# Kernel optimization log

Hardware: AMD Instinct MI355X
Metric: run time of the kernel (lower is better)

The kernel has to match this reference:

```python
import jax, jax.numpy as jnp
import numpy as np

B, T, D = 4, 2048, 768
H = 12
DH = D // H
DFF = 3072
EPS = 1e-5


def _layernorm(x, g, b):
    mu = jnp.mean(x, axis=-1, keepdims=True)
    var = jnp.var(x, axis=-1, keepdims=True)
    return (x - mu) * jax.lax.rsqrt(var + EPS) * g + b


def setup_inputs() -> dict:
    key = jax.random.key(0)
    ks = jax.random.split(key, 12)
    s = lambda fan_in: 1.0 / np.sqrt(fan_in)
    return {
        "x": jax.random.normal(ks[0], (B, T, D), dtype=jnp.float32),
        "ln1_g": jnp.ones((D,), jnp.float32),
        "ln1_b": jnp.zeros((D,), jnp.float32),
        "w_qkv": jax.random.uniform(ks[1], (D, 3 * D), jnp.float32, -s(D), s(D)),
        "b_qkv": jax.random.uniform(ks[2], (3 * D,), jnp.float32, -s(D), s(D)),
        "w_proj": jax.random.uniform(ks[3], (D, D), jnp.float32, -s(D), s(D)),
        "b_proj": jax.random.uniform(ks[4], (D,), jnp.float32, -s(D), s(D)),
        "ln2_g": jnp.ones((D,), jnp.float32),
        "ln2_b": jnp.zeros((D,), jnp.float32),
        "w_ff1": jax.random.uniform(ks[5], (D, DFF), jnp.float32, -s(D), s(D)),
        "b_ff1": jax.random.uniform(ks[6], (DFF,), jnp.float32, -s(D), s(D)),
        "w_ff2": jax.random.uniform(ks[7], (DFF, D), jnp.float32, -s(DFF), s(DFF)),
        "b_ff2": jax.random.uniform(ks[8], (D,), jnp.float32, -s(DFF), s(DFF)),
    }


def reference(x, ln1_g, ln1_b, w_qkv, b_qkv, w_proj, b_proj,
              ln2_g, ln2_b, w_ff1, b_ff1, w_ff2, b_ff2):
    # --- attention sublayer ---
    h = _layernorm(x, ln1_g, ln1_b)
    qkv = h @ w_qkv + b_qkv                       # [B,T,3D]
    q, k, v = jnp.split(qkv, 3, axis=-1)
    q = q.reshape(B, T, H, DH).transpose(0, 2, 1, 3)  # [B,H,T,DH]
    k = k.reshape(B, T, H, DH).transpose(0, 2, 1, 3)
    v = v.reshape(B, T, H, DH).transpose(0, 2, 1, 3)
    att = jnp.einsum('bhqd,bhkd->bhqk', q, k) / jnp.sqrt(jnp.float32(DH))
    causal = jnp.tril(jnp.ones((T, T), dtype=bool))
    att = jnp.where(causal, att, -jnp.inf)
    att = jax.nn.softmax(att, axis=-1)
    out = jnp.einsum('bhqk,bhkd->bhqd', att, v)    # [B,H,T,DH]
    out = out.transpose(0, 2, 1, 3).reshape(B, T, D)
    x = x + out @ w_proj + b_proj
    # --- MLP sublayer ---
    h2 = _layernorm(x, ln2_g, ln2_b)
    h2 = jax.nn.gelu(h2 @ w_ff1 + b_ff1, approximate=False)
    x = x + h2 @ w_ff2 + b_ff2
    return x
```

## Files before the change

### kernel.cpp

```cpp
#include <hip/hip_runtime.h>
#include <cstdint>
#include <cstddef>

typedef unsigned short u16;
typedef unsigned int u32;
typedef __attribute__((ext_vector_type(8))) short s16x8;
typedef __attribute__((ext_vector_type(4))) float f32x4;

#define NB 4
#define NT 2048
#define ND 768
#define NH 12
#define NDH 64
#define NFF 3072
#define NM (NB*NT)

__device__ __forceinline__ u16 f2b(float f){
  union { float f; unsigned u; } c; c.f = f;
  unsigned r = c.u + 0x7fffu + ((c.u >> 16) & 1u);
  return (u16)(r >> 16);
}

__device__ __forceinline__ f32x4 mfma16(s16x8 a, s16x8 b, f32x4 c){
  return __builtin_amdgcn_mfma_f32_16x16x32_bf16(a, b, c, 0, 0, 0);
}

__device__ __forceinline__ void stage16(u16* lds, const u16* g){
  __builtin_amdgcn_global_load_lds(
      (const __attribute__((address_space(1))) unsigned int*)g,
      (__attribute__((address_space(3))) unsigned int*)lds,
      16, 0, 0);
}

__device__ __forceinline__ float gelu_f(float v){
  const float x = v * 0.70710678118654752f;
  const float ax = fabsf(x);
  const float t = 1.f / (1.f + 0.3275911f * ax);
  const float y = t * (0.254829592f + t * (-0.284496736f + t * (1.421413741f
                + t * (-1.453152027f + t * 1.061405429f))));
  float er = 1.f - y * __expf(-ax * ax);
  er = copysignf(er, x);
  return 0.5f * v * (1.f + er);
}

__global__ __launch_bounds__(256) void transpose_bf16(
    const float* __restrict__ in, u16* __restrict__ out, int K, int N)
{
  __shared__ float tile[32][33];
  const int n0 = blockIdx.x * 32, k0 = blockIdx.y * 32;
  const int tx = threadIdx.x, ty = threadIdx.y;
  #pragma unroll
  for (int i = 0; i < 32; i += 8)
    tile[ty + i][tx] = in[(size_t)(k0 + ty + i) * N + n0 + tx];
  __syncthreads();
  #pragma unroll
  for (int i = 0; i < 32; i += 8)
    out[(size_t)(n0 + ty + i) * K + k0 + tx] = f2b(tile[tx][ty + i]);
}

__global__ __launch_bounds__(256) void ln_kernel(
    const float* __restrict__ x, const float* __restrict__ g,
    const float* __restrict__ b, u16* __restrict__ out)
{
  const int row = blockIdx.x;
  const int t = threadIdx.x;
  const float* xr = x + (size_t)row * ND;
  float v0 = xr[t], v1 = xr[t + 256], v2 = xr[t + 512];
  float s = v0 + v1 + v2;
  float ss = v0*v0 + v1*v1 + v2*v2;
  #pragma unroll
  for (int o = 32; o; o >>= 1) { s += __shfl_xor(s, o, 64); ss += __shfl_xor(ss, o, 64); }
  __shared__ float red[8];
  const int w = t >> 6;
  if ((t & 63) == 0) { red[w] = s; red[4 + w] = ss; }
  __syncthreads();
  s  = red[0] + red[1] + red[2] + red[3];
  ss = red[4] + red[5] + red[6] + red[7];
  const float mu = s * (1.f / ND);
  const float var = ss * (1.f / ND) - mu * mu;
  const float rinv = rsqrtf(var + 1e-5f);
  u16* orow = out + (size_t)row * ND;
  orow[t]       = f2b((v0 - mu) * rinv * g[t]       + b[t]);
  orow[t + 256] = f2b((v1 - mu) * rinv * g[t + 256] + b[t + 256]);
  orow[t + 512] = f2b((v2 - mu) * rinv * g[t + 512] + b[t + 512]);
}

template<int EPI>
__global__ __launch_bounds__(512,6) void gemm_bt(
    const u16* __restrict__ A, const u16* __restrict__ Bt,
    const float* __restrict__ bias, const float* __restrict__ res,
    void* __restrict__ o0, void* __restrict__ o1, void* __restrict__ o2,
    const int M, const int N, const int K)
{
  __shared__ u16 As[128 * 32];
  __shared__ u16 Bs[128 * 32];
  const int tid = threadIdx.x;
  const int lane = tid & 63, wid = tid >> 6;
  const int wr = wid >> 1, wc = wid & 1;
  const int lg = lane >> 4, lm = lane & 15;

  const int nwg = gridDim.x * gridDim.y;
  int bid = blockIdx.y * gridDim.x + blockIdx.x;
  bid = (bid & 7) * (nwg >> 3) + (bid >> 3);
  const int bm = (bid & 63) * 128, bn = (bid >> 6) * 128;

  f32x4 acc[2][4] = {};

  const int srow = tid >> 2;
  const int schunk = (tid & 3) ^ ((tid >> 3) & 3);
  const u16* ApT = A  + (size_t)(bm + srow) * K + schunk * 8;
  const u16* BpT = Bt + (size_t)(bn + srow) * K + schunk * 8;
  const int woff = wid * 512;
  const int fswz = (lm >> 1) & 3;

  const int nt = K >> 5;
  for (int t = 0; t < nt; ++t) {
    const int k0 = t << 5;
    __syncthreads();
    stage16(&As[woff], ApT + k0);
    stage16(&Bs[woff], BpT + k0);
    __syncthreads();
    s16x8 af[2], bf[4];
    #pragma unroll
    for (int i = 0; i < 2; i++)
      af[i] = *(const s16x8*)&As[(wr * 32 + i * 16 + lm) * 32 + ((lg ^ fswz) * 8)];
    #pragma unroll
    for (int j = 0; j < 4; j++)
      bf[j] = *(const s16x8*)&Bs[(wc * 64 + j * 16 + lm) * 32 + ((lg ^ fswz) * 8)];
    #pragma unroll
    for (int i = 0; i < 2; i++)
      #pragma unroll
      for (int j = 0; j < 4; j++)
        acc[i][j] = mfma16(af[i], bf[j], acc[i][j]);
  }

  #pragma unroll
  for (int i = 0; i < 2; i++)
    #pragma unroll
    for (int j = 0; j < 4; j++) {
      const int col = bn + wc * 64 + j * 16 + lm;
      const float bb = bias[col];
      #pragma unroll
      for (int r = 0; r < 4; r++) {
        const int row = bm + wr * 32 + i * 16 + lg * 4 + r;
        float v = acc[i][j][r] + bb;
        if (EPI == 0) {
          u16* dst; int rem;
          if (col < ND)            { dst = (u16*)o0; rem = col; v *= 0.125f; }
          else if (col < 2 * ND)   { dst = (u16*)o1; rem = col - ND; }
          else                     { dst = (u16*)o2; rem = col - 2 * ND; }
          const int hh = rem >> 6, dh = rem & 63;
          const int bb2 = row >> 11, tt = row & 2047;
          dst[(((size_t)bb2 * NH + hh) * NT + tt) * NDH + dh] = f2b(v);
        } else if (EPI == 1) {
          ((float*)o0)[(size_t)row * ND + col] = v + res[(size_t)row * ND + col];
        } else if (EPI == 2) {
          ((u16*)o0)[(size_t)row * NFF + col] = f2b(gelu_f(v));
        } else {
          ((float*)o0)[(size_t)row * ND + col] = v + res[(size_t)row * ND + col];
        }
      }
    }
}

__global__ __launch_bounds__(256,2) void attn_kernel(
    const u16* __restrict__ Q, const u16* __restrict__ Kg,
    const u16* __restrict__ V, u16* __restrict__ O)
{
  const int pairIdx = blockIdx.x;
  const int bh = blockIdx.y;
  const int b = bh / NH, h = bh % NH;
  const int tid = threadIdx.x;
  const int lane = tid & 63, w = tid >> 6;
  const int lg = lane >> 4, lm = lane & 15;
  const int sr = tid >> 3;
  const int sc = (tid & 7) * 8;

  __shared__ u16 Ks[64 * 64];
  __shared__ u16 Vt[64 * 64];
  __shared__ u16 Ps[4][16 * 64];

  const u16* Qb = Q  + (size_t)bh * NT * NDH;
  const u16* Kb = Kg + (size_t)bh * NT * NDH;
  const u16* Vb = V  + (size_t)bh * NT * NDH;

  for (int half = 0; half < 2; ++half) {
    const int si = half ? (31 - pairIdx) : pairIdx;
    const int q0 = si * 64;
    const int ktmax = si;

    const s16x8 qf0 = *(const s16x8*)&Qb[(size_t)(q0 + w * 16 + lm) * NDH + lg * 8];
    const s16x8 qf1 = *(const s16x8*)&Qb[(size_t)(q0 + w * 16 + lm) * NDH + 32 + lg * 8];

    f32x4 oacc[4] = {};
    float m = -INFINITY, l = 0.f;

    s16x8 kva = *(const s16x8*)&Kb[(size_t)sr * NDH + sc];
    s16x8 kvb = *(const s16x8*)&Kb[(size_t)(sr + 32) * NDH + sc];
    s16x8 vva = *(const s16x8*)&Vb[(size_t)sr * NDH + sc];
    s16x8 vvb = *(const s16x8*)&Vb[(size_t)(sr + 32) * NDH + sc];

    for (int kt = 0; kt <= ktmax; ++kt) {
      __syncthreads();
      *(s16x8*)&Ks[sr * 64 + (sc ^ ((sr & 7) << 3))] = kva;
      *(s16x8*)&Ks[(sr + 32) * 64 + (sc ^ ((sr & 7) << 3))] = kvb;
      #pragma unroll
      for (int e = 0; e < 8; ++e)
        Vt[(sc + e) * 64 + (sr ^ ((tid & 7) << 3))] = (u16)vva[e];
      #pragma unroll
      for (int e = 0; e < 8; ++e)
        Vt[(sc + e) * 64 + ((sr + 32) ^ ((tid & 7) << 3))] = (u16)vvb[e];
      __syncthreads();

      if (kt < ktmax) {
        const u16* Kn = Kb + (size_t)(kt + 1) * 64 * NDH;
        const u16* Vn = Vb + (size_t)(kt + 1) * 64 * NDH;
        kva = *(const s16x8*)&Kn[(size_t)sr * NDH + sc];
        kvb = *(const s16x8*)&Kn[(size_t)(sr + 32) * NDH + sc];
        vva = *(const s16x8*)&Vn[(size_t)sr * NDH + sc];
        vvb = *(const s16x8*)&Vn[(size_t)(sr + 32) * NDH + sc];
      }

      f32x4 sv[4];
      #pragma unroll
      for (int n = 0; n < 4; ++n) {
        const int krow = (n * 16 + lm) * 64;
        const int swz = (lm & 7) << 3;
        s16x8 kf0 = *(const s16x8*)&Ks[krow + ((lg * 8) ^ swz)];
        s16x8 kf1 = *(const s16x8*)&Ks[krow + ((32 + lg * 8) ^ swz)];
        f32x4 s4 = {};
        s4 = mfma16(kf0, qf0, s4);
        s4 = mfma16(kf1, qf1, s4);
        sv[n] = s4;
      }

      if (kt == ktmax) {
        #pragma unroll
        for (int n = 0; n < 4; ++n)
          #pragma unroll
          for (int r = 0; r < 4; ++r)
            if (n * 16 + lg * 4 + r > w * 16 + lm) sv[n][r] = -INFINITY;
      }

      float mx = -INFINITY;
      #pragma unroll
      for (int n = 0; n < 4; ++n)
        #pragma unroll
        for (int r = 0; r < 4; ++r) mx = fmaxf(mx, sv[n][r]);
      mx = fmaxf(mx, __shfl_xor(mx, 16));
      mx = fmaxf(mx, __shfl_xor(mx, 32));
      const float mnew = fmaxf(m, mx);
      const float alpha = __expf(m - mnew);
      m = mnew;

      float rs = 0.f;
      u32 pk[4][2];
      #pragma unroll
      for (int n = 0; n < 4; ++n) {
        const float p0 = __expf(sv[n][0] - mnew);
        const float p1 = __expf(sv[n][1] - mnew);
        const float p2 = __expf(sv[n][2] - mnew);
        const float p3 = __expf(sv[n][3] - mnew);
        rs += (p0 + p1) + (p2 + p3);
        pk[n][0] = (u32)f2b(p0) | ((u32)f2b(p1) << 16);
        pk[n][1] = (u32)f2b(p2) | ((u32)f2b(p3) << 16);
      }
      rs += __shfl_xor(rs, 16);
      rs += __shfl_xor(rs, 32);
      l = l * alpha + rs;

      #pragma unroll
      for (int n = 0; n < 4; ++n) {
        const int idx0 = lm * 64 + ((n * 16 + lg * 4) ^ ((lm & 7) << 3));
        *(u32*)&Ps[w][idx0] = pk[n][0];
        *(u32*)&Ps[w][idx0 + 2] = pk[n][1];
      }

      float av[4];
      #pragma unroll
      for (int r = 0; r < 4; ++r) av[r] = __shfl(alpha, lg * 4 + r);
      #pragma unroll
      for (int d = 0; d < 4; ++d)
        #pragma unroll
        for (int r = 0; r < 4; ++r) oacc[d][r] *= av[r];

      #pragma unroll
      for (int kh = 0; kh < 2; ++kh) {
        const s16x8 pf = *(const s16x8*)&Ps[w][lm * 64 + ((kh * 32 + lg * 8) ^ ((lm & 7) << 3))];
        #pragma unroll
        for (int dt = 0; dt < 4; ++dt) {
          const int g = (2 * dt + (lm >> 3)) & 7;
          const s16x8 vf = *(const s16x8*)&Vt[(dt * 16 + lm) * 64 + (((kh * 4 + lg) ^ g) << 3)];
          oacc[dt] = mfma16(pf, vf, oacc[dt]);
        }
      }
    }

    float lv[4];
    #pragma unroll
    for (int r = 0; r < 4; ++r) lv[r] = 1.f / __shfl(l, lg * 4 + r);
    #pragma unroll
    for (int dt = 0; dt < 4; ++dt)
      #pragma unroll
      for (int r = 0; r < 4; ++r) {
        const int qg = q0 + w * 16 + lg * 4 + r;
        O[((size_t)b * NT + qg) * ND + h * NDH + dt * 16 + lm] = f2b(oacc[dt][r] * lv[r]);
      }
  }
}

extern "C" void kernel_launch(void* const* d_in, const int* in_sizes, int n_in,
                              void* d_out, int out_size, void* d_ws, size_t ws_size,
                              hipStream_t stream)
{
  const float* x      = (const float*)d_in[0];
  const float* ln1_g  = (const float*)d_in[1];
  const float* ln1_b  = (const float*)d_in[2];
  const float* w_qkv  = (const float*)d_in[3];
  const float* b_qkv  = (const float*)d_in[4];
  const float* w_proj = (const float*)d_in[5];
  const float* b_proj = (const float*)d_in[6];
  const float* ln2_g  = (const float*)d_in[7];
  const float* ln2_b  = (const float*)d_in[8];
  const float* w_ff1  = (const float*)d_in[9];
  const float* b_ff1  = (const float*)d_in[10];
  const float* w_ff2  = (const float*)d_in[11];
  const float* b_ff2  = (const float*)d_in[12];

  char* ws = (char*)d_ws;
  u16*   wt_qkv = (u16*)(ws + 0);
  u16*   wt_proj= (u16*)(ws + 3538944);
  u16*   wt_ff1 = (u16*)(ws + 4718592);
  u16*   wt_ff2 = (u16*)(ws + 9437184);
  u16*   hbuf   = (u16*)(ws + 14155776);
  u16*   qbuf   = (u16*)(ws + 26738688);
  u16*   kbuf   = (u16*)(ws + 39321600);
  u16*   vbuf   = (u16*)(ws + 51904512);
  u16*   aobuf  = (u16*)(ws + 64487424);
  float* x1     = (float*)(ws + 77070336);
  u16*   h2buf  = (u16*)(ws + 102236160);
  u16*   ff1buf = hbuf;

  transpose_bf16<<<dim3(2304/32,  768/32), dim3(32,8), 0, stream>>>(w_qkv,  wt_qkv,  768, 2304);
  transpose_bf16<<<dim3( 768/32,  768/32), dim3(32,8), 0, stream>>>(w_proj, wt_proj, 768,  768);
  transpose_bf16<<<dim3(3072/32,  768/32), dim3(32,8), 0, stream>>>(w_ff1,  wt_ff1,  768, 3072);
  transpose_bf16<<<dim3( 768/32, 3072/32), dim3(32,8), 0, stream>>>(w_ff2,  wt_ff2, 3072,  768);

  ln_kernel<<<NM, 256, 0, stream>>>(x, ln1_g, ln1_b, hbuf);
  gemm_bt<0><<<dim3(NM/128, 2304/128), 512, 0, stream>>>(hbuf, wt_qkv, b_qkv, nullptr,
                                                         qbuf, kbuf, vbuf, NM, 2304, ND);
  attn_kernel<<<dim3(16, NB*NH), 256, 0, stream>>>(qbuf, kbuf, vbuf, aobuf);
  gemm_bt<1><<<dim3(NM/128, ND/128), 512, 0, stream>>>(aobuf, wt_proj, b_proj, x,
                                                       x1, nullptr, nullptr, NM, ND, ND);
  ln_kernel<<<NM, 256, 0, stream>>>(x1, ln2_g, ln2_b, h2buf);
  gemm_bt<2><<<dim3(NM/128, NFF/128), 512, 0, stream>>>(h2buf, wt_ff1, b_ff1, nullptr,
                                                        ff1buf, nullptr, nullptr, NM, NFF, ND);
  gemm_bt<3><<<dim3(NM/128, ND/128), 512, 0, stream>>>(ff1buf, wt_ff2, b_ff2, x1,
                                                       d_out, nullptr, nullptr, NM, ND, NFF);
}
```

Baseline: 328.5 us.

## Triple-buffer GEMM LDS with async prefetch, 256-thread blocks, BM=64 for N=768 GEMMs

The GEMM moves from single-buffered LDS with two barriers per K-step to a three-stage ring buffer. Tiles are prefetched two steps ahead, and explicit vmcnt waits plus a single barrier per iteration let global loads overlap MFMA work. Blocks shrink to 256 threads, so each wave computes a larger register tile. The narrow projection and FF2 GEMMs use a 64-row tile to get more blocks. The XCD-aware block remap is dropped, and the attention grid axes are swapped so that heads vary fastest. The added LDS and register pressure may reduce occupancy, and the hand-written vmcnt counts depend on how stage16 issues its loads.

```diff
diff --git a/kernel.cpp b/kernel.cpp
--- a/kernel.cpp
+++ b/kernel.cpp
@@ -85,64 +85,85 @@
   orow[t + 512] = f2b((v2 - mu) * rinv * g[t + 512] + b[t + 512]);
 }
 
-template<int EPI>
-__global__ __launch_bounds__(512,6) void gemm_bt(
+template<int EPI, int BM>
+__global__ __launch_bounds__(256, (BM == 128) ? 3 : 4) void gemm_bt(
     const u16* __restrict__ A, const u16* __restrict__ Bt,
     const float* __restrict__ bias, const float* __restrict__ res,
     void* __restrict__ o0, void* __restrict__ o1, void* __restrict__ o2,
     const int M, const int N, const int K)
 {
-  __shared__ u16 As[128 * 32];
-  __shared__ u16 Bs[128 * 32];
+  constexpr int MI = BM / 64;
+  __shared__ u16 As[3][BM * 32];
+  __shared__ u16 Bs[3][128 * 32];
   const int tid = threadIdx.x;
   const int lane = tid & 63, wid = tid >> 6;
   const int wr = wid >> 1, wc = wid & 1;
   const int lg = lane >> 4, lm = lane & 15;
-
-  const int nwg = gridDim.x * gridDim.y;
-  int bid = blockIdx.y * gridDim.x + blockIdx.x;
-  bid = (bid & 7) * (nwg >> 3) + (bid >> 3);
-  const int bm = (bid & 63) * 128, bn = (bid >> 6) * 128;
-
-  f32x4 acc[2][4] = {};
+  const int bm = blockIdx.x * BM, bn = blockIdx.y * 128;
+
+  f32x4 acc[2 * MI][4] = {};
 
   const int srow = tid >> 2;
   const int schunk = (tid & 3) ^ ((tid >> 3) & 3);
   const u16* ApT = A  + (size_t)(bm + srow) * K + schunk * 8;
   const u16* BpT = Bt + (size_t)(bn + srow) * K + schunk * 8;
+  const size_t rs64 = (size_t)64 * K;
   const int woff = wid * 512;
   const int fswz = (lm >> 1) & 3;
 
   const int nt = K >> 5;
+
+  #pragma unroll
+  for (int p = 0; p < 2; ++p) {
+    const int k0 = p << 5;
+    stage16(&As[p][woff], ApT + k0);
+    if (BM == 128) stage16(&As[p][woff + 2048], ApT + rs64 + k0);
+    stage16(&Bs[p][woff],        BpT + k0);
+    stage16(&Bs[p][woff + 2048], BpT + rs64 + k0);
+  }
+
   for (int t = 0; t < nt; ++t) {
-    const int k0 = t << 5;
-    __syncthreads();
-    stage16(&As[woff], ApT + k0);
-    stage16(&Bs[woff], BpT + k0);
-    __syncthreads();
-    s16x8 af[2], bf[4];
-    #pragma unroll
-    for (int i = 0; i < 2; i++)
-      af[i] = *(const s16x8*)&As[(wr * 32 + i * 16 + lm) * 32 + ((lg ^ fswz) * 8)];
+    if (t < nt - 1) {
+      if (BM == 128) asm volatile("s_waitcnt vmcnt(4)" ::: "memory");
+      else           asm volatile("s_waitcnt vmcnt(3)" ::: "memory");
+    } else {
+      asm volatile("s_waitcnt vmcnt(0)" ::: "memory");
+    }
+    __builtin_amdgcn_s_barrier();
+    __builtin_amdgcn_sched_barrier(0);
+    if (t + 2 < nt) {
+      const int k0 = (t + 2) << 5;
+      const int wb = (t + 2) % 3;
+      stage16(&As[wb][woff], ApT + k0);
+      if (BM == 128) stage16(&As[wb][woff + 2048], ApT + rs64 + k0);
+      stage16(&Bs[wb][woff],        BpT + k0);
+      stage16(&Bs[wb][woff + 2048], BpT + rs64 + k0);
+    }
+    __builtin_amdgcn_sched_barrier(0);
+    const int rb = t % 3;
+    s16x8 af[2 * MI], bf[4];
+    #pragma unroll
+    for (int i = 0; i < 2 * MI; i++)
+      af[i] = *(const s16x8*)&As[rb][(wr * (BM / 2) + i * 16 + lm) * 32 + ((lg ^ fswz) * 8)];
     #pragma unroll
     for (int j = 0; j < 4; j++)
-      bf[j] = *(const s16x8*)&Bs[(wc * 64 + j * 16 + lm) * 32 + ((lg ^ fswz) * 8)];
-    #pragma unroll
-    for (int i = 0; i < 2; i++)
+      bf[j] = *(const s16x8*)&Bs[rb][(wc * 64 + j * 16 + lm) * 32 + ((lg ^ fswz) * 8)];
+    #pragma unroll
+    for (int i = 0; i < 2 * MI; i++)
       #pragma unroll
       for (int j = 0; j < 4; j++)
         acc[i][j] = mfma16(af[i], bf[j], acc[i][j]);
   }
 
   #pragma unroll
-  for (int i = 0; i < 2; i++)
+  for (int i = 0; i < 2 * MI; i++)
     #pragma unroll
     for (int j = 0; j < 4; j++) {
       const int col = bn + wc * 64 + j * 16 + lm;
       const float bb = bias[col];
       #pragma unroll
       for (int r = 0; r < 4; r++) {
-        const int row = bm + wr * 32 + i * 16 + lg * 4 + r;
+        const int row = bm + wr * (BM / 2) + i * 16 + lg * 4 + r;
         float v = acc[i][j][r] + bb;
         if (EPI == 0) {
           u16* dst; int rem;
@@ -167,8 +188,8 @@
     const u16* __restrict__ Q, const u16* __restrict__ Kg,
     const u16* __restrict__ V, u16* __restrict__ O)
 {
-  const int pairIdx = blockIdx.x;
-  const int bh = blockIdx.y;
+  const int pairIdx = blockIdx.y;
+  const int bh = blockIdx.x;
   const int b = bh / NH, h = bh % NH;
   const int tid = threadIdx.x;
   const int lane = tid & 63, w = tid >> 6;
@@ -347,14 +368,14 @@
   transpose_bf16<<<dim3( 768/32, 3072/32), dim3(32,8), 0, stream>>>(w_ff2,  wt_ff2, 3072,  768);
 
   ln_kernel<<<NM, 256, 0, stream>>>(x, ln1_g, ln1_b, hbuf);
-  gemm_bt<0><<<dim3(NM/128, 2304/128), 512, 0, stream>>>(hbuf, wt_qkv, b_qkv, nullptr,
-                                                         qbuf, kbuf, vbuf, NM, 2304, ND);
-  attn_kernel<<<dim3(16, NB*NH), 256, 0, stream>>>(qbuf, kbuf, vbuf, aobuf);
-  gemm_bt<1><<<dim3(NM/128, ND/128), 512, 0, stream>>>(aobuf, wt_proj, b_proj, x,
-                                                       x1, nullptr, nullptr, NM, ND, ND);
+  gemm_bt<0,128><<<dim3(NM/128, 2304/128), 256, 0, stream>>>(hbuf, wt_qkv, b_qkv, nullptr,
+                                                             qbuf, kbuf, vbuf, NM, 2304, ND);
+  attn_kernel<<<dim3(NB*NH, 16), 256, 0, stream>>>(qbuf, kbuf, vbuf, aobuf);
+  gemm_bt<1,64><<<dim3(NM/64, ND/128), 256, 0, stream>>>(aobuf, wt_proj, b_proj, x,
+                                                         x1, nullptr, nullptr, NM, ND, ND);
   ln_kernel<<<NM, 256, 0, stream>>>(x1, ln2_g, ln2_b, h2buf);
-  gemm_bt<2><<<dim3(NM/128, NFF/128), 512, 0, stream>>>(h2buf, wt_ff1, b_ff1, nullptr,
-                                                        ff1buf, nullptr, nullptr, NM, NFF, ND);
-  gemm_bt<3><<<dim3(NM/128, ND/128), 512, 0, stream>>>(ff1buf, wt_ff2, b_ff2, x1,
-                                                       d_out, nullptr, nullptr, NM, ND, NFF);
-}
+  gemm_bt<2,128><<<dim3(NM/128, NFF/128), 256, 0, stream>>>(h2buf, wt_ff1, b_ff1, nullptr,
+                                                            ff1buf, nullptr, nullptr, NM, NFF, ND);
+  gemm_bt<3,64><<<dim3(NM/64, ND/128), 256, 0, stream>>>(ff1buf, wt_ff2, b_ff2, x1,
+                                                         d_out, nullptr, nullptr, NM, ND, NFF);
+}
```

After: 293.3 us. 10.7% less time.
